# Optimization experiments

Measured on AMD Instinct MI355X. Metric: run time of the kernel, lower is better.

The kernel has to match this reference:

```python
import jax, jax.numpy as jnp
from jax import lax
import numpy as np

EPS = 1e-5  # torch BatchNorm2d default eps


def _conv(x, w, b):
    # NCHW conv, stride 1, 'same' padding (matches nn.Conv2d(padding='same'))
    y = lax.conv_general_dilated(x, w, (1, 1), 'SAME',
                                 dimension_numbers=('NCHW', 'OIHW', 'NCHW'))
    return y + b[None, :, None, None]


def _bn(x, g, b, m, v):
    # eval-mode BatchNorm2d using running stats
    s = g * lax.rsqrt(v + EPS)
    return x * s[None, :, None, None] + (b - m * s)[None, :, None, None]


def _pool(x):
    # MaxPool2d(2, 2)
    return lax.reduce_window(x, -jnp.inf, lax.max, (1, 1, 2, 2), (1, 1, 2, 2), 'VALID')


def setup_inputs() -> dict:
    key = jax.random.key(0)
    ks = list(jax.random.split(key, 16))
    B, H, W = 64, 128, 128
    chans = [1, 32, 64, 96]
    R, C_LRLC, HL, WL = 4, 128, 16, 16
    FC1, NCLS = 512, 10

    def nrm(k, shape, fan_in):
        return jax.random.normal(k, shape, jnp.float32) / np.float32(np.sqrt(fan_in))

    inp = {"x": jax.random.normal(ks[0], (B, 1, H, W), jnp.float32)}
    for i in range(3):
        ci, co = chans[i], chans[i + 1]
        inp[f"conv{i+1}_w"] = nrm(ks[1 + i], (co, ci, 3, 3), ci * 9)
        inp[f"conv{i+1}_b"] = jnp.zeros((co,), jnp.float32)
        inp[f"bn{i+1}_g"] = jnp.ones((co,), jnp.float32)
        inp[f"bn{i+1}_b"] = jnp.zeros((co,), jnp.float32)
        inp[f"bn{i+1}_m"] = 0.1 * jax.random.normal(ks[4 + i], (co,), jnp.float32)
        inp[f"bn{i+1}_v"] = jax.random.uniform(ks[7 + i], (co,), jnp.float32, 0.5, 1.5)
    # LRLC basis filters: R basis kernels stacked along out-channel dim
    inp["basis_w"] = nrm(ks[10], (R * C_LRLC, chans[-1], 3, 3), chans[-1] * 9)
    inp["basis_b"] = jnp.zeros((R, C_LRLC), jnp.float32)  # per-rank bias basis
    # OuterCombiningWeights: row/col logits, softmax over rank per location
    inp["cw_h"] = 0.1 * jax.random.normal(ks[11], (HL, R), jnp.float32)
    inp["cw_w"] = 0.1 * jax.random.normal(ks[12], (WL, R), jnp.float32)
    inp["fc1_w"] = nrm(ks[13], (FC1, HL * WL * C_LRLC), HL * WL * C_LRLC)
    inp["fc1_b"] = jnp.zeros((FC1,), jnp.float32)
    inp["fc2_w"] = nrm(ks[14], (NCLS, FC1), FC1)
    inp["fc2_b"] = jnp.zeros((NCLS,), jnp.float32)
    return inp


def reference(x, conv1_w, conv1_b, bn1_g, bn1_b, bn1_m, bn1_v,
              conv2_w, conv2_b, bn2_g, bn2_b, bn2_m, bn2_v,
              conv3_w, conv3_b, bn3_g, bn3_b, bn3_m, bn3_v,
              basis_w, basis_b, cw_h, cw_w, fc1_w, fc1_b, fc2_w, fc2_b):
    blocks = ((conv1_w, conv1_b, bn1_g, bn1_b, bn1_m, bn1_v),
              (conv2_w, conv2_b, bn2_g, bn2_b, bn2_m, bn2_v),
              (conv3_w, conv3_b, bn3_g, bn3_b, bn3_m, bn3_v))
    for cw_, cb_, g_, b_, m_, v_ in blocks:  # conv -> BN -> ReLU -> pool
        x = _pool(jax.nn.relu(_bn(_conv(x, cw_, cb_), g_, b_, m_, v_)))

    R, C = basis_b.shape
    # combining weights: softmax over rank at each (h, w)
    cw = jax.nn.softmax(cw_h[:, None, :] + cw_w[None, :, :], axis=-1)  # (HL, WL, R)
    # R basis convolutions in one call, then per-location low-rank combine
    y = lax.conv_general_dilated(x, basis_w, (1, 1), 'SAME',
                                 dimension_numbers=('NCHW', 'OIHW', 'NCHW'))
    B, _, HL, WL = y.shape
    y = y.reshape(B, R, C, HL, WL)
    out = jnp.einsum('brchw,hwr->bchw', y, cw)
    out = out + jnp.einsum('hwr,rc->chw', cw, basis_b)[None]  # low-rank spatial bias
    out = jax.nn.relu(out)
    out = out.reshape(B, -1)
    out = jax.nn.relu(out @ fc1_w.T + fc1_b)
    return out @ fc2_w.T + fc2_b
```

## Files before the change

kernel.cpp:

```cpp
#include <hip/hip_runtime.h>
#include <hip/hip_bf16.h>

#define EPS 1e-5f

typedef short s16x8 __attribute__((ext_vector_type(8)));
typedef float f32x4 __attribute__((ext_vector_type(4)));

__device__ __forceinline__ unsigned short f2bf(float f) {
    unsigned u = __float_as_uint(f);
    u += 0x7fffu + ((u >> 16) & 1u);
    return (unsigned short)(u >> 16);
}

__global__ __launch_bounds__(256) void repack_conv1(
    const float* __restrict__ x,
    const float* __restrict__ c1w, const float* __restrict__ c1b,
    const float* __restrict__ b1g, const float* __restrict__ b1b,
    const float* __restrict__ b1m, const float* __restrict__ b1v,
    const float* __restrict__ c2w, const float* __restrict__ c3w,
    const float* __restrict__ bw,
    unsigned short* __restrict__ act1,
    unsigned short* __restrict__ wp2S, unsigned short* __restrict__ wp3F,
    unsigned short* __restrict__ wpL3)
{
    const int tid = threadIdx.x;
    if (blockIdx.x >= 4096) {
        int idx = (blockIdx.x - 4096) * 256 + tid;
        if (idx < 18432) {
            int ch = idx >> 3, e = idx & 7;
            int co = ch / 36, rem = ch % 36;
            int s = rem >> 2, slot = rem & 3;
            int g = slot ^ ((co >> 1) & 3);
            int ci = g * 8 + e;
            wp2S[idx] = f2bf(c2w[(co * 32 + ci) * 9 + s]);
        } else if (idx < 73728) {
            int i = idx - 18432;
            int e    = i & 7;
            int lane = (i >> 3) & 63;
            int f    = i >> 9;
            int cg   = f % 6;
            int t2   = f / 6;
            int kk   = t2 & 1;
            int s    = t2 >> 1;
            int col = lane & 15, quad = lane >> 4;
            int co = cg * 16 + col;
            int ci = (kk * 4 + quad) * 8 + e;
            wp3F[i] = f2bf(c3w[(co * 64 + ci) * 9 + s]);
        } else if (idx < 516096) {
            int i = idx - 73728;
            int e    = i & 7;
            int lane = (i >> 3) & 63;
            int fk   = i >> 9;
            int kk   = fk % 3;
            int t    = fk / 3;
            int j    = t & 1;
            int rp   = (t >> 1) & 1;
            int g    = (t >> 2) & 1;
            int cbk  = (t >> 3) & 3;
            int s    = t >> 5;
            int col = lane & 15, quad = lane >> 4;
            int cog = (rp * 2 + j) * 128 + cbk * 32 + g * 16 + col;
            int ci  = (kk * 4 + quad) * 8 + e;
            wpL3[i] = f2bf(bw[(cog * 96 + ci) * 9 + s]);
        }
        return;
    }

    __shared__ float xs[4][132];
    __shared__ float wfs[320];

    const int bid = blockIdx.x;
    const int b = bid >> 6, ph = bid & 63;

    for (int i = tid; i < 4 * 132; i += 256) ((float*)xs)[i] = 0.f;
    for (int i = tid; i < 320; i += 256) {
        int co = i / 10, k = i % 10;
        float scl = b1g[co] * rsqrtf(b1v[co] + EPS);
        wfs[i] = (k < 9) ? c1w[co * 9 + k] * scl
                         : (c1b[co] - b1m[co]) * scl + b1b[co];
    }
    __syncthreads();
    const int row0 = 2 * ph - 1;
    for (int i = tid; i < 4 * 128; i += 256) {
        int r = i >> 7, c = i & 127;
        int gr = row0 + r;
        if (gr >= 0 && gr < 128)
            xs[r][c + 1] = x[(size_t)b * 16384 + gr * 128 + c];
    }
    __syncthreads();

    const int pw = tid & 63, wavei = tid >> 6;
    float pr[4][4];
    #pragma unroll
    for (int rr = 0; rr < 4; ++rr) {
        float2 u0 = *(const float2*)&xs[rr][2 * pw];
        float2 u1 = *(const float2*)&xs[rr][2 * pw + 2];
        pr[rr][0] = u0.x; pr[rr][1] = u0.y; pr[rr][2] = u1.x; pr[rr][3] = u1.y;
    }

    const float* wb = wfs + wavei * 80;
    s16x8 res;
    #pragma unroll
    for (int c8 = 0; c8 < 8; ++c8) {
        const float* wv = wb + c8 * 10;
        float a00 = 0.f, a01 = 0.f, a10 = 0.f, a11 = 0.f;
        #pragma unroll
        for (int ky = 0; ky < 3; ++ky)
            #pragma unroll
            for (int kx = 0; kx < 3; ++kx) {
                float wk = wv[ky * 3 + kx];
                a00 = fmaf(wk, pr[ky][kx],         a00);
                a01 = fmaf(wk, pr[ky][kx + 1],     a01);
                a10 = fmaf(wk, pr[ky + 1][kx],     a10);
                a11 = fmaf(wk, pr[ky + 1][kx + 1], a11);
            }
        float o = fmaxf(fmaxf(fmaxf(a00, a01), fmaxf(a10, a11)) + wv[9], 0.f);
        res[c8] = (short)f2bf(o);
    }
    *(s16x8*)(act1 + (((size_t)(b * 64 + ph)) * 64 + pw) * 32 + wavei * 8) = res;
}

__global__ __launch_bounds__(256) void conv2_mfma(
    const unsigned short* __restrict__ xin,
    const unsigned short* __restrict__ wp2S,
    const float* __restrict__ cbv, const float* __restrict__ gg,
    const float* __restrict__ bnb, const float* __restrict__ mm,
    const float* __restrict__ vv,
    unsigned short* __restrict__ out)
{
    constexpr int CI = 32, CO = 64, W = 64, WT = 66, CG = 4;
    constexpr int ASZ = 4 * WT * CI * 2;
    constexpr int BSZ = 9 * CO * CI * 2;
    constexpr int PH2 = 32, HPX = 4;

    __shared__ __align__(16) unsigned char sm[ASZ + BSZ];

    const int tid = threadIdx.x;
    const int wave = tid >> 6, lane = tid & 63;
    const int quad = lane >> 4, col = lane & 15;
    const int wm = wave;

    const int xcd  = blockIdx.x & 7;
    const int slot = blockIdx.x >> 3;
    const int hp = xcd * HPX + (slot % HPX);
    const int b  = slot / HPX;

    constexpr int NCHA = 4 * WT * CG;
    for (int ch = tid; ch < NCHA; ch += 256) {
        int r    = ch / (WT * CG);
        int rem  = ch % (WT * CG);
        int wp   = rem / CG;
        int slot_ = rem % CG;
        int g = slot_ ^ ((wp >> 1) & 3);
        int h = hp * 2 - 1 + r;
        int w = wp - 1;
        s16x8 val = {};
        if (h >= 0 && h < W && w >= 0 && w < W)
            val = *(const s16x8*)(xin + (((size_t)(b * W + h) * W + w) * CI + g * 8));
        *(s16x8*)(sm + ch * 16) = val;
    }
    for (int ch = tid; ch < 2304; ch += 256)
        *(s16x8*)(sm + ASZ + ch * 16) = *(const s16x8*)(wp2S + ch * 8);
    __syncthreads();

    f32x4 acc[2][4];
    #pragma unroll
    for (int i = 0; i < 2; ++i)
        #pragma unroll
        for (int j = 0; j < 4; ++j) acc[i][j] = (f32x4){0.f, 0.f, 0.f, 0.f};

    #pragma unroll
    for (int s = 0; s < 9; ++s) {
        const int dy = s / 3, dx = s % 3;
        const int g = quad;
        s16x8 a[2];
        #pragma unroll
        for (int mi = 0; mi < 2; ++mi) {
            int wp = wm * 16 + col + dx;
            int r  = mi + dy;
            int addr = (r * WT + wp) * (CI * 2) + ((g ^ ((wp >> 1) & 3)) << 4);
            a[mi] = *(const s16x8*)(sm + addr);
        }
        #pragma unroll
        for (int nf = 0; nf < 4; ++nf) {
            int co_l = nf * 16 + col;
            int row = co_l * 9 + s;
            int addr = ASZ + row * (CI * 2) + ((g ^ ((co_l >> 1) & 3)) << 4);
            s16x8 bf = *(const s16x8*)(sm + addr);
            acc[0][nf] = __builtin_amdgcn_mfma_f32_16x16x32_bf16(a[0], bf, acc[0][nf], 0, 0, 0);
            acc[1][nf] = __builtin_amdgcn_mfma_f32_16x16x32_bf16(a[1], bf, acc[1][nf], 0, 0, 0);
        }
    }

    #pragma unroll
    for (int nf = 0; nf < 4; ++nf) {
        int co = nf * 16 + col;
        float scl = gg[co] * rsqrtf(vv[co] + EPS);
        float sh  = (cbv[co] - mm[co]) * scl + bnb[co];
        #pragma unroll
        for (int pr = 0; pr < 2; ++pr) {
            float y0 = fmaf(acc[0][nf][2 * pr],     scl, sh);
            float y1 = fmaf(acc[0][nf][2 * pr + 1], scl, sh);
            float y2 = fmaf(acc[1][nf][2 * pr],     scl, sh);
            float y3 = fmaf(acc[1][nf][2 * pr + 1], scl, sh);
            float o = fmaxf(fmaxf(fmaxf(y0, y1), fmaxf(y2, y3)), 0.f);
            int pw = wm * 8 + quad * 2 + pr;
            out[((size_t)(b * PH2 + hp) * PH2 + pw) * CO + co] = f2bf(o);
        }
    }
}

__global__ __launch_bounds__(256) void conv3_mfma(
    const unsigned short* __restrict__ xin,
    const unsigned short* __restrict__ wp3F,
    const float* __restrict__ cbv, const float* __restrict__ gg,
    const float* __restrict__ bnb, const float* __restrict__ mm,
    const float* __restrict__ vv,
    unsigned short* __restrict__ out)
{
    constexpr int CI = 64, CO = 96, W = 32, WT = 34, CG = 8;
    constexpr int ASZ = 4 * WT * CI * 2;
    constexpr int PH2 = 16, HPX = 2;

    __shared__ __align__(16) unsigned char sm[ASZ];

    const int tid = threadIdx.x;
    const int wave = tid >> 6, lane = tid & 63;
    const int quad = lane >> 4, col = lane & 15;
    const int wm = wave & 1, wn = wave >> 1;

    const int xcd  = blockIdx.x & 7;
    const int slot = blockIdx.x >> 3;
    const int hp = xcd * HPX + (slot % HPX);
    const int b  = slot / HPX;

    constexpr int NCHA = 4 * WT * CG;
    for (int ch = tid; ch < NCHA; ch += 256) {
        int r    = ch / (WT * CG);
        int rem  = ch % (WT * CG);
        int wp   = rem / CG;
        int slot_ = rem % CG;
        int g = slot_ ^ (wp & 7);
        int h = hp * 2 - 1 + r;
        int w = wp - 1;
        s16x8 val = {};
        if (h >= 0 && h < W && w >= 0 && w < W)
            val = *(const s16x8*)(xin + (((size_t)(b * W + h) * W + w) * CI + g * 8));
        *(s16x8*)(sm + ch * 16) = val;
    }
    __syncthreads();

    f32x4 acc[2][3];
    #pragma unroll
    for (int i = 0; i < 2; ++i)
        #pragma unroll
        for (int j = 0; j < 3; ++j) acc[i][j] = (f32x4){0.f, 0.f, 0.f, 0.f};

    for (int s = 0; s < 9; ++s) {
        const int dy = s / 3, dx = s % 3;
        s16x8 bf[3][2];
        #pragma unroll
        for (int nf = 0; nf < 3; ++nf)
            #pragma unroll
            for (int kk = 0; kk < 2; ++kk) {
                int fidx = (((s * 2 + kk) * 6) + wn * 3 + nf) * 512 + lane * 8;
                bf[nf][kk] = *(const s16x8*)(wp3F + fidx);
            }
        #pragma unroll
        for (int kk = 0; kk < 2; ++kk) {
            const int g = kk * 4 + quad;
            s16x8 a[2];
            #pragma unroll
            for (int mi = 0; mi < 2; ++mi) {
                int wp = wm * 16 + col + dx;
                int r  = mi + dy;
                int addr = (r * WT + wp) * (CI * 2) + ((g ^ (wp & 7)) << 4);
                a[mi] = *(const s16x8*)(sm + addr);
            }
            #pragma unroll
            for (int nf = 0; nf < 3; ++nf) {
                acc[0][nf] = __builtin_amdgcn_mfma_f32_16x16x32_bf16(a[0], bf[nf][kk], acc[0][nf], 0, 0, 0);
                acc[1][nf] = __builtin_amdgcn_mfma_f32_16x16x32_bf16(a[1], bf[nf][kk], acc[1][nf], 0, 0, 0);
            }
        }
    }

    #pragma unroll
    for (int nf = 0; nf < 3; ++nf) {
        int co = (wn * 3 + nf) * 16 + col;
        float scl = gg[co] * rsqrtf(vv[co] + EPS);
        float sh  = (cbv[co] - mm[co]) * scl + bnb[co];
        #pragma unroll
        for (int pr = 0; pr < 2; ++pr) {
            float y0 = fmaf(acc[0][nf][2 * pr],     scl, sh);
            float y1 = fmaf(acc[0][nf][2 * pr + 1], scl, sh);
            float y2 = fmaf(acc[1][nf][2 * pr],     scl, sh);
            float y3 = fmaf(acc[1][nf][2 * pr + 1], scl, sh);
            float o = fmaxf(fmaxf(fmaxf(y0, y1), fmaxf(y2, y3)), 0.f);
            int pw = wm * 8 + quad * 2 + pr;
            out[((size_t)(b * PH2 + hp) * PH2 + pw) * CO + co] = f2bf(o);
        }
    }
}

__global__ __launch_bounds__(512) void lrlc_mfma4(
    const unsigned short* __restrict__ xin,
    const unsigned short* __restrict__ wpk3,
    const float* __restrict__ bbias,
    const float* __restrict__ cwh, const float* __restrict__ cww,
    unsigned short* __restrict__ actB)
{
    constexpr int CI = 96, WT = 18, NR = 10, CG = 12;
    constexpr int ASZ = NR * WT * CI * 2;
    __shared__ __align__(16) unsigned char sm[ASZ];
    __shared__ float cwt[256][4];

    const int tid = threadIdx.x;
    const int wave = tid >> 6, lane = tid & 63;
    const int quad = lane >> 4, col = lane & 15;
    const int wm = wave & 1;
    const int g  = (wave >> 1) & 1;
    const int rp = wave >> 2;

    const int cbk = blockIdx.x & 3;
    const int mb  = (blockIdx.x >> 2) & 1;
    const int b   = blockIdx.x >> 3;

    if (tid < 256) {
        int h = tid >> 4, w = tid & 15;
        float e[4], mx = -1e30f;
        #pragma unroll
        for (int r = 0; r < 4; ++r) { e[r] = cwh[h * 4 + r] + cww[w * 4 + r]; mx = fmaxf(mx, e[r]); }
        float se = 0.f;
        #pragma unroll
        for (int r = 0; r < 4; ++r) { e[r] = expf(e[r] - mx); se += e[r]; }
        float inv = 1.f / se;
        #pragma unroll
        for (int r = 0; r < 4; ++r) cwt[tid][r] = e[r] * inv;
    }

    constexpr int NCHA = NR * WT * CG;
    for (int ch = tid; ch < NCHA; ch += 512) {
        int r    = ch / (WT * CG);
        int rem  = ch % (WT * CG);
        int wp   = rem / CG, slot = rem % CG;
        int gg_ = slot ^ ((wp >> 1) & 3);
        int h = mb * 8 + r - 1;
        int w = wp - 1;
        s16x8 val = {};
        if (h >= 0 && h < 16 && w >= 0 && w < 16)
            val = *(const s16x8*)(xin + (((size_t)(b * 16 + h) * 16 + w) * CI + gg_ * 8));
        *(s16x8*)(sm + ch * 16) = val;
    }
    __syncthreads();

    f32x4 acc[4][2];
    #pragma unroll
    for (int i = 0; i < 4; ++i)
        #pragma unroll
        for (int j = 0; j < 2; ++j) acc[i][j] = (f32x4){0.f, 0.f, 0.f, 0.f};

    const int tbase = ((cbk * 2 + g) * 2 + rp);
    for (int s = 0; s < 9; ++s) {
        const int dy = s / 3, dx = s % 3;
        s16x8 bf[2][3];
        #pragma unroll
        for (int j = 0; j < 2; ++j)
            #pragma unroll
            for (int kk = 0; kk < 3; ++kk) {
                int fidx = ((s * 32 + tbase * 2 + j) * 3 + kk) * 512 + lane * 8;
                bf[j][kk] = *(const s16x8*)(wpk3 + fidx);
            }
        #pragma unroll
        for (int kk = 0; kk < 3; ++kk) {
            const int gg = kk * 4 + quad;
            s16x8 a[4];
            #pragma unroll
            for (int mi = 0; mi < 4; ++mi) {
                int mf = wm * 4 + mi;
                int r  = mf + dy;
                int wp = col + dx;
                int addr = (r * WT + wp) * (CI * 2) + ((gg ^ ((wp >> 1) & 3)) << 4);
                a[mi] = *(const s16x8*)(sm + addr);
            }
            #pragma unroll
            for (int mi = 0; mi < 4; ++mi)
                #pragma unroll
                for (int j = 0; j < 2; ++j)
                    acc[mi][j] = __builtin_amdgcn_mfma_f32_16x16x32_bf16(
                        a[mi], bf[j][kk], acc[mi][j], 0, 0, 0);
        }
    }
    __syncthreads();

    float* ldo = (float*)sm;
    {
        const int c_lo = g * 16 + col;
        const int cg   = cbk * 32 + c_lo;
        float bbA = bbias[(rp * 2 + 0) * 128 + cg];
        float bbB = bbias[(rp * 2 + 1) * 128 + cg];
        #pragma unroll
        for (int mi = 0; mi < 4; ++mi) {
            int mf = wm * 4 + mi;
            #pragma unroll
            for (int rg = 0; rg < 4; ++rg) {
                int hwl = mf * 16 + quad * 4 + rg;
                int hwg = mb * 128 + hwl;
                float o = cwt[hwg][rp * 2]     * (acc[mi][0][rg] + bbA)
                        + cwt[hwg][rp * 2 + 1] * (acc[mi][1][rg] + bbB);
                ldo[(rp * 128 + hwl) * 33 + c_lo] = o;
            }
        }
    }
    __syncthreads();
    {
        int cl = tid >> 4;
        int sg = tid & 15;
        size_t base = (size_t)b * 32768 + (cbk * 32 + cl) * 256 + mb * 128 + sg * 8;
        s16x8 v;
        #pragma unroll
        for (int i = 0; i < 8; ++i) {
            int hw = sg * 8 + i;
            float o = ldo[hw * 33 + cl] + ldo[(128 + hw) * 33 + cl];
            v[i] = (short)f2bf(fmaxf(o, 0.f));
        }
        *(s16x8*)(actB + base) = v;
    }
}

__global__ __launch_bounds__(256) void fc1_stream(
    const unsigned short* __restrict__ actB,
    const float* __restrict__ w,
    float* __restrict__ partial)
{
    __shared__ __align__(16) unsigned short Wl[64 * 256];
    __shared__ __align__(16) unsigned short Al[64 * 256];

    const int tid = threadIdx.x;
    const int wave = tid >> 6, lane = tid & 63;
    const int quad = lane >> 4, col = lane & 15;
    const int wm = wave & 1, wn = wave >> 1;
    const int xcd  = blockIdx.x & 7;
    const int slot = blockIdx.x >> 3;
    const int ks = xcd * 16 + (slot >> 3);
    const int jt = slot & 7;
    const int k0 = ks * 256;

    const int rt  = tid >> 2;
    const int seg = tid & 3;

    const float* wsrc = w + (size_t)(jt * 64 + rt) * 32768 + k0 + seg * 64;
    const unsigned short* asrc = actB + (size_t)rt * 32768 + k0 + seg * 64;

    #pragma unroll
    for (int u = 0; u < 8; ++u) {
        float4 f0 = *(const float4*)(wsrc + u * 8);
        float4 f1 = *(const float4*)(wsrc + u * 8 + 4);
        s16x8 av = *(const s16x8*)(asrc + u * 8);
        s16x8 v;
        v[0] = (short)f2bf(f0.x); v[1] = (short)f2bf(f0.y);
        v[2] = (short)f2bf(f0.z); v[3] = (short)f2bf(f0.w);
        v[4] = (short)f2bf(f1.x); v[5] = (short)f2bf(f1.y);
        v[6] = (short)f2bf(f1.z); v[7] = (short)f2bf(f1.w);
        int phys = (seg * 8 + u) ^ (rt & 7);
        *(s16x8*)(Wl + rt * 256 + phys * 8) = v;
        *(s16x8*)(Al + rt * 256 + phys * 8) = av;
    }
    __syncthreads();

    f32x4 acc[2][2];
    #pragma unroll
    for (int i = 0; i < 2; ++i)
        #pragma unroll
        for (int j = 0; j < 2; ++j) acc[i][j] = (f32x4){0.f, 0.f, 0.f, 0.f};

    #pragma unroll
    for (int kk = 0; kk < 8; ++kk) {
        const int gg = kk * 4 + quad;
        s16x8 a[2], bb[2];
        #pragma unroll
        for (int mf = 0; mf < 2; ++mf) {
            int j_l = wm * 32 + mf * 16 + col;
            a[mf] = *(const s16x8*)(Wl + j_l * 256 + ((gg ^ (j_l & 7)) << 3));
        }
        #pragma unroll
        for (int bg = 0; bg < 2; ++bg) {
            int b_l = wn * 32 + bg * 16 + col;
            bb[bg] = *(const s16x8*)(Al + b_l * 256 + ((gg ^ (b_l & 7)) << 3));
        }
        #pragma unroll
        for (int mf = 0; mf < 2; ++mf)
            #pragma unroll
            for (int bg = 0; bg < 2; ++bg)
                acc[mf][bg] = __builtin_amdgcn_mfma_f32_16x16x32_bf16(
                    a[mf], bb[bg], acc[mf][bg], 0, 0, 0);
    }
    #pragma unroll
    for (int mf = 0; mf < 2; ++mf)
        #pragma unroll
        for (int bg = 0; bg < 2; ++bg)
            #pragma unroll
            for (int r = 0; r < 4; ++r) {
                int j = jt * 64 + wm * 32 + mf * 16 + quad * 4 + r;
                int b = wn * 32 + bg * 16 + col;
                partial[((size_t)ks * 512 + j) * 64 + b] = acc[mf][bg][r];
            }
}

__global__ __launch_bounds__(256) void fc1_reduce6(
    const float* __restrict__ partial, const float* __restrict__ bias,
    float* __restrict__ out)
{
    int idx = blockIdx.x * 256 + threadIdx.x;
    int b = idx & 63, j = idx >> 6;
    float a = bias[j];
    #pragma unroll 16
    for (int ks = 0; ks < 128; ++ks)
        a += partial[((size_t)ks * 512 + j) * 64 + b];
    out[b * 512 + j] = fmaxf(a, 0.f);
}

__global__ __launch_bounds__(320) void fc2_w(
    const float* __restrict__ xin,
    const float* __restrict__ w,
    const float* __restrict__ bias,
    float* __restrict__ out)
{
    const int b = blockIdx.x;
    const int tid = threadIdx.x;
    const int n = tid >> 5, l = tid & 31;
    const float* xr = xin + b * 512 + l * 16;
    const float* wr = w + n * 512 + l * 16;
    float s = 0.f;
    #pragma unroll
    for (int u = 0; u < 4; ++u) {
        float4 xv = *(const float4*)(xr + u * 4);
        float4 wv = *(const float4*)(wr + u * 4);
        s = fmaf(xv.x, wv.x, s); s = fmaf(xv.y, wv.y, s);
        s = fmaf(xv.z, wv.z, s); s = fmaf(xv.w, wv.w, s);
    }
    #pragma unroll
    for (int off = 16; off > 0; off >>= 1)
        s += __shfl_xor(s, off, 32);
    if (l == 0) out[b * 10 + n] = s + bias[n];
}

extern "C" void kernel_launch(void* const* d_in, const int* in_sizes, int n_in,
                              void* d_out, int out_size, void* d_ws, size_t ws_size,
                              hipStream_t stream) {
    const float* x   = (const float*)d_in[0];
    const float* c1w = (const float*)d_in[1];  const float* c1b = (const float*)d_in[2];
    const float* b1g = (const float*)d_in[3];  const float* b1b = (const float*)d_in[4];
    const float* b1m = (const float*)d_in[5];  const float* b1v = (const float*)d_in[6];
    const float* c2w = (const float*)d_in[7];  const float* c2b = (const float*)d_in[8];
    const float* b2g = (const float*)d_in[9];  const float* b2b = (const float*)d_in[10];
    const float* b2m = (const float*)d_in[11]; const float* b2v = (const float*)d_in[12];
    const float* c3w = (const float*)d_in[13]; const float* c3b = (const float*)d_in[14];
    const float* b3g = (const float*)d_in[15]; const float* b3b = (const float*)d_in[16];
    const float* b3m = (const float*)d_in[17]; const float* b3v = (const float*)d_in[18];
    const float* bw  = (const float*)d_in[19]; const float* bb  = (const float*)d_in[20];
    const float* cwh = (const float*)d_in[21]; const float* cww = (const float*)d_in[22];
    const float* f1w = (const float*)d_in[23]; const float* f1b = (const float*)d_in[24];
    const float* f2w = (const float*)d_in[25]; const float* f2b = (const float*)d_in[26];
    float* out = (float*)d_out;

    char* ws = (char*)d_ws;
    unsigned short* act1 = (unsigned short*)(ws + 0);
    unsigned short* act2 = (unsigned short*)(ws + 16777216);
    unsigned short* act3 = (unsigned short*)(ws + 0);
    unsigned short* actB = (unsigned short*)(ws + 4194304);
    float*          part = (float*)(ws + 8388608);
    float*          fc1o = (float*)(ws + 0);
    unsigned short* wp2S = (unsigned short*)(ws + 25165824);
    unsigned short* wp3F = (unsigned short*)(ws + 25202688);
    unsigned short* wpL3 = (unsigned short*)(ws + 25313280);

    repack_conv1<<<6112, 256, 0, stream>>>(x, c1w, c1b, b1g, b1b, b1m, b1v,
                                           c2w, c3w, bw, act1, wp2S, wp3F, wpL3);

    conv2_mfma<<<2048, 256, 0, stream>>>(act1, wp2S, c2b, b2g, b2b, b2m, b2v, act2);

    conv3_mfma<<<1024, 256, 0, stream>>>(act2, wp3F, c3b, b3g, b3b, b3m, b3v, act3);

    lrlc_mfma4<<<512, 512, 0, stream>>>(act3, wpL3, bb, cwh, cww, actB);

    fc1_stream<<<1024, 256, 0, stream>>>(actB, f1w, part);
    fc1_reduce6<<<128, 256, 0, stream>>>(part, f1b, fc1o);
    fc2_w<<<64, 320, 0, stream>>>(fc1o, f2w, f2b, out);
}
```

Measured before the change: 97.63 us.

## Deepen fc1 K-slices with register-prefetched chunks, simplify conv staging indexing

fc1 now gives each block a 512-wide K slice in two 256-wide chunks, with all global loads for both chunks issued into registers up front. This halves the partial-sum buffer and the work in the reduction kernel, and is meant to raise memory-level parallelism while the fc1 weights stream in. The cost is much higher register pressure, an extra barrier between chunks, and half as many blocks. The conv2/conv3 activation staging loops are also restructured per row, replacing div/mod indexing with shifts.

```diff
diff --git a/kernel.cpp b/kernel.cpp
--- a/kernel.cpp
+++ b/kernel.cpp
@@ -145,19 +145,19 @@
     const int hp = xcd * HPX + (slot % HPX);
     const int b  = slot / HPX;
 
-    constexpr int NCHA = 4 * WT * CG;
-    for (int ch = tid; ch < NCHA; ch += 256) {
-        int r    = ch / (WT * CG);
-        int rem  = ch % (WT * CG);
-        int wp   = rem / CG;
-        int slot_ = rem % CG;
-        int g = slot_ ^ ((wp >> 1) & 3);
+    #pragma unroll
+    for (int r = 0; r < 4; ++r) {
         int h = hp * 2 - 1 + r;
-        int w = wp - 1;
-        s16x8 val = {};
-        if (h >= 0 && h < W && w >= 0 && w < W)
-            val = *(const s16x8*)(xin + (((size_t)(b * W + h) * W + w) * CI + g * 8));
-        *(s16x8*)(sm + ch * 16) = val;
+        bool hok = (h >= 0) && (h < W);
+        for (int i = tid; i < WT * CG; i += 256) {
+            int wp = i >> 2, slot_ = i & 3;
+            int g = slot_ ^ ((wp >> 1) & 3);
+            int w = wp - 1;
+            s16x8 val = {};
+            if (hok && w >= 0 && w < W)
+                val = *(const s16x8*)(xin + (((size_t)(b * W + h) * W + w) * CI + g * 8));
+            *(s16x8*)(sm + (r * WT * CG + i) * 16) = val;
+        }
     }
     for (int ch = tid; ch < 2304; ch += 256)
         *(s16x8*)(sm + ASZ + ch * 16) = *(const s16x8*)(wp2S + ch * 8);
@@ -234,19 +234,19 @@
     const int hp = xcd * HPX + (slot % HPX);
     const int b  = slot / HPX;
 
-    constexpr int NCHA = 4 * WT * CG;
-    for (int ch = tid; ch < NCHA; ch += 256) {
-        int r    = ch / (WT * CG);
-        int rem  = ch % (WT * CG);
-        int wp   = rem / CG;
-        int slot_ = rem % CG;
-        int g = slot_ ^ (wp & 7);
+    #pragma unroll
+    for (int r = 0; r < 4; ++r) {
         int h = hp * 2 - 1 + r;
-        int w = wp - 1;
-        s16x8 val = {};
-        if (h >= 0 && h < W && w >= 0 && w < W)
-            val = *(const s16x8*)(xin + (((size_t)(b * W + h) * W + w) * CI + g * 8));
-        *(s16x8*)(sm + ch * 16) = val;
+        bool hok = (h >= 0) && (h < W);
+        for (int i = tid; i < WT * CG; i += 256) {
+            int wp = i >> 3, slot_ = i & 7;
+            int g = slot_ ^ (wp & 7);
+            int w = wp - 1;
+            s16x8 val = {};
+            if (hok && w >= 0 && w < W)
+                val = *(const s16x8*)(xin + (((size_t)(b * W + h) * W + w) * CI + g * 8));
+            *(s16x8*)(sm + (r * WT * CG + i) * 16) = val;
+        }
     }
     __syncthreads();
 
@@ -428,7 +428,7 @@
     }
 }
 
-__global__ __launch_bounds__(256) void fc1_stream(
+__global__ __launch_bounds__(256) void fc1_deep(
     const unsigned short* __restrict__ actB,
     const float* __restrict__ w,
     float* __restrict__ partial)
@@ -442,9 +442,9 @@
     const int wm = wave & 1, wn = wave >> 1;
     const int xcd  = blockIdx.x & 7;
     const int slot = blockIdx.x >> 3;
-    const int ks = xcd * 16 + (slot >> 3);
+    const int ks = xcd * 8 + (slot >> 3);
     const int jt = slot & 7;
-    const int k0 = ks * 256;
+    const int k0 = ks * 512;
 
     const int rt  = tid >> 2;
     const int seg = tid & 3;
@@ -452,21 +452,15 @@
     const float* wsrc = w + (size_t)(jt * 64 + rt) * 32768 + k0 + seg * 64;
     const unsigned short* asrc = actB + (size_t)rt * 32768 + k0 + seg * 64;
 
-    #pragma unroll
-    for (int u = 0; u < 8; ++u) {
-        float4 f0 = *(const float4*)(wsrc + u * 8);
-        float4 f1 = *(const float4*)(wsrc + u * 8 + 4);
-        s16x8 av = *(const s16x8*)(asrc + u * 8);
-        s16x8 v;
-        v[0] = (short)f2bf(f0.x); v[1] = (short)f2bf(f0.y);
-        v[2] = (short)f2bf(f0.z); v[3] = (short)f2bf(f0.w);
-        v[4] = (short)f2bf(f1.x); v[5] = (short)f2bf(f1.y);
-        v[6] = (short)f2bf(f1.z); v[7] = (short)f2bf(f1.w);
-        int phys = (seg * 8 + u) ^ (rt & 7);
-        *(s16x8*)(Wl + rt * 256 + phys * 8) = v;
-        *(s16x8*)(Al + rt * 256 + phys * 8) = av;
-    }
-    __syncthreads();
+    float4 pw0[2][8], pw1[2][8]; s16x8 pa[2][8];
+    #pragma unroll
+    for (int c = 0; c < 2; ++c)
+        #pragma unroll
+        for (int u = 0; u < 8; ++u) {
+            pw0[c][u] = *(const float4*)(wsrc + c * 256 + u * 8);
+            pw1[c][u] = *(const float4*)(wsrc + c * 256 + u * 8 + 4);
+            pa[c][u]  = *(const s16x8*)(asrc + c * 256 + u * 8);
+        }
 
     f32x4 acc[2][2];
     #pragma unroll
@@ -475,25 +469,41 @@
         for (int j = 0; j < 2; ++j) acc[i][j] = (f32x4){0.f, 0.f, 0.f, 0.f};
 
     #pragma unroll
-    for (int kk = 0; kk < 8; ++kk) {
-        const int gg = kk * 4 + quad;
-        s16x8 a[2], bb[2];
-        #pragma unroll
-        for (int mf = 0; mf < 2; ++mf) {
-            int j_l = wm * 32 + mf * 16 + col;
-            a[mf] = *(const s16x8*)(Wl + j_l * 256 + ((gg ^ (j_l & 7)) << 3));
-        }
-        #pragma unroll
-        for (int bg = 0; bg < 2; ++bg) {
-            int b_l = wn * 32 + bg * 16 + col;
-            bb[bg] = *(const s16x8*)(Al + b_l * 256 + ((gg ^ (b_l & 7)) << 3));
-        }
-        #pragma unroll
-        for (int mf = 0; mf < 2; ++mf)
-            #pragma unroll
-            for (int bg = 0; bg < 2; ++bg)
-                acc[mf][bg] = __builtin_amdgcn_mfma_f32_16x16x32_bf16(
-                    a[mf], bb[bg], acc[mf][bg], 0, 0, 0);
+    for (int c = 0; c < 2; ++c) {
+        if (c) __syncthreads();
+        #pragma unroll
+        for (int u = 0; u < 8; ++u) {
+            s16x8 v;
+            v[0] = (short)f2bf(pw0[c][u].x); v[1] = (short)f2bf(pw0[c][u].y);
+            v[2] = (short)f2bf(pw0[c][u].z); v[3] = (short)f2bf(pw0[c][u].w);
+            v[4] = (short)f2bf(pw1[c][u].x); v[5] = (short)f2bf(pw1[c][u].y);
+            v[6] = (short)f2bf(pw1[c][u].z); v[7] = (short)f2bf(pw1[c][u].w);
+            int phys = (seg * 8 + u) ^ (rt & 7);
+            *(s16x8*)(Wl + rt * 256 + phys * 8) = v;
+            *(s16x8*)(Al + rt * 256 + phys * 8) = pa[c][u];
+        }
+        __syncthreads();
+        #pragma unroll
+        for (int kk = 0; kk < 8; ++kk) {
+            const int gg = kk * 4 + quad;
+            s16x8 a[2], bb[2];
+            #pragma unroll
+            for (int mf = 0; mf < 2; ++mf) {
+                int j_l = wm * 32 + mf * 16 + col;
+                a[mf] = *(const s16x8*)(Wl + j_l * 256 + ((gg ^ (j_l & 7)) << 3));
+            }
+            #pragma unroll
+            for (int bg = 0; bg < 2; ++bg) {
+                int b_l = wn * 32 + bg * 16 + col;
+                bb[bg] = *(const s16x8*)(Al + b_l * 256 + ((gg ^ (b_l & 7)) << 3));
+            }
+            #pragma unroll
+            for (int mf = 0; mf < 2; ++mf)
+                #pragma unroll
+                for (int bg = 0; bg < 2; ++bg)
+                    acc[mf][bg] = __builtin_amdgcn_mfma_f32_16x16x32_bf16(
+                        a[mf], bb[bg], acc[mf][bg], 0, 0, 0);
+        }
     }
     #pragma unroll
     for (int mf = 0; mf < 2; ++mf)
@@ -507,15 +517,15 @@
             }
 }
 
-__global__ __launch_bounds__(256) void fc1_reduce6(
+__global__ __launch_bounds__(256) void fc1_reduce4(
     const float* __restrict__ partial, const float* __restrict__ bias,
     float* __restrict__ out)
 {
     int idx = blockIdx.x * 256 + threadIdx.x;
     int b = idx & 63, j = idx >> 6;
     float a = bias[j];
-    #pragma unroll 16
-    for (int ks = 0; ks < 128; ++ks)
+    #pragma unroll 8
+    for (int ks = 0; ks < 64; ++ks)
         a += partial[((size_t)ks * 512 + j) * 64 + b];
     out[b * 512 + j] = fmaxf(a, 0.f);
 }
@@ -584,7 +594,7 @@
 
     lrlc_mfma4<<<512, 512, 0, stream>>>(act3, wpL3, bb, cwh, cww, actB);
 
-    fc1_stream<<<1024, 256, 0, stream>>>(actB, f1w, part);
-    fc1_reduce6<<<128, 256, 0, stream>>>(part, f1b, fc1o);
+    fc1_deep<<<512, 256, 0, stream>>>(actB, f1w, part);
+    fc1_reduce4<<<128, 256, 0, stream>>>(part, f1b, fc1o);
     fc2_w<<<64, 320, 0, stream>>>(fc1o, f2w, f2b, out);
 }
```

Result: slower. 101.2 us (+3.6%).
